# Kernel optimization log

Hardware: AMD Instinct MI355X
Metric: run time of the kernel (lower is better)

## Reference

```python
import jax, jax.numpy as jnp
import numpy as np

D = 768          # wav2vec2-base hidden size
H = 4            # cross-attn heads
HD = D // H
B = 8
N = 1024         # w2v sequence length (target length)
T = 2000         # raw CQCC frames
N_GAT = 3
NUM_CLASSES = 2


def _p(key, shape, scale=0.02):
    return jax.random.normal(key, shape, dtype=jnp.float32) * scale


def layer_norm(x, g, b, eps=1e-5):
    m = x.mean(-1, keepdims=True)
    v = x.var(-1, keepdims=True)
    return (x - m) * jax.lax.rsqrt(v + eps) * g + b


def gelu(x):
    return jax.nn.gelu(x, approximate=False)


def conv1d(x, w, b):
    # x [B,C,T], w [O,I,K], padding=1 (same)
    y = jax.lax.conv_general_dilated(x, w, (1,), [(1, 1)], dimension_numbers=('NCH', 'OIH', 'NCH'))
    return y + b[None, :, None]


def batchnorm(x, g, b, m, v, eps=1e-5):
    # eval-mode BatchNorm1d on [B,C,T]
    return (x - m[None, :, None]) * jax.lax.rsqrt(v[None, :, None] + eps) * g[None, :, None] + b[None, :, None]


def interp_linear(x, target_len):
    # torch F.interpolate(mode='linear', align_corners=False); x [B,T,D] -> [B,target_len,D]
    t_in = x.shape[1]
    pos = (jnp.arange(target_len, dtype=jnp.float32) + 0.5) * (t_in / target_len) - 0.5
    pos = jnp.clip(pos, 0.0, t_in - 1.0)
    lo = jnp.floor(pos).astype(jnp.int32)
    hi = jnp.minimum(lo + 1, t_in - 1)
    w = (pos - lo.astype(jnp.float32))[None, :, None]
    return x[:, lo] * (1.0 - w) + x[:, hi] * w


def mha(q, k, v, in_w, in_b, out_w, out_b):
    # torch nn.MultiheadAttention, batch_first=True
    bb, nq, _ = q.shape
    nk = k.shape[1]
    wq, wk, wv = in_w[:D], in_w[D:2 * D], in_w[2 * D:]
    bq, bk, bv = in_b[:D], in_b[D:2 * D], in_b[2 * D:]
    qh = (q @ wq.T + bq).reshape(bb, nq, H, HD).transpose(0, 2, 1, 3)
    kh = (k @ wk.T + bk).reshape(bb, nk, H, HD).transpose(0, 2, 1, 3)
    vh = (v @ wv.T + bv).reshape(bb, nk, H, HD).transpose(0, 2, 1, 3)
    scores = jnp.einsum('bhqd,bhkd->bhqk', qh, kh) * (1.0 / np.sqrt(HD))
    alpha = jax.nn.softmax(scores, axis=-1)
    o = jnp.einsum('bhqk,bhkd->bhqd', alpha, vh).transpose(0, 2, 1, 3).reshape(bb, nq, D)
    return o @ out_w.T + out_b


def graph_attn(x, fc_w, fc_b, a_w, a_b):
    # GAT score on concat([h_i, h_j]) decomposes additively: e_ij = a_i.h_i + a_j.h_j + b
    h = x @ fc_w.T + fc_b                      # [B,N,D]
    s_i = h @ a_w[:D]                          # [B,N]
    s_j = h @ a_w[D:]                          # [B,N]
    e = s_i[:, :, None] + s_j[:, None, :] + a_b  # [B,N,N]
    alpha = jax.nn.softmax(e, axis=-1)
    return jnp.einsum('bij,bjd->bid', alpha, h)


def _forward(w2v, cqcc, conv1_w, conv1_b, bn1_g, bn1_b, bn1_m, bn1_v,
             conv2_w, conv2_b, bn2_g, bn2_b, bn2_m, bn2_v, pos_embed,
             lnq_g, lnq_b, lnkv_g, lnkv_b,
             a1_in_w, a1_in_b, a1_out_w, a1_out_b,
             a2_in_w, a2_in_b, a2_out_w, a2_out_b,
             gat_fc_w, gat_fc_b, gat_a_w, gat_a_b, gln_g, gln_b,
             clf_w1, clf_b1, clf_w2, clf_b2):
    # CQCC conv stack
    x = gelu(batchnorm(conv1d(cqcc, conv1_w, conv1_b), bn1_g, bn1_b, bn1_m, bn1_v))
    x = gelu(batchnorm(conv1d(x, conv2_w, conv2_b), bn2_g, bn2_b, bn2_m, bn2_v))  # [B,D,T]
    cq = interp_linear(x.transpose(0, 2, 1), w2v.shape[1])  # [B,N,D]
    # shared positional encoding
    n = w2v.shape[1]
    w = w2v + pos_embed[:, :n]
    cq = cq + pos_embed[:, :n]
    # bidirectional cross attention (norm_q / norm_kv shared across directions)
    out1 = mha(layer_norm(cq, lnq_g, lnq_b), layer_norm(w, lnkv_g, lnkv_b),
               layer_norm(w, lnkv_g, lnkv_b), a1_in_w, a1_in_b, a1_out_w, a1_out_b)
    out2 = mha(layer_norm(w, lnq_g, lnq_b), layer_norm(cq, lnkv_g, lnkv_b),
               layer_norm(cq, lnkv_g, lnkv_b), a2_in_w, a2_in_b, a2_out_w, a2_out_b)
    x = out1 + out2
    # 3 residual graph-attention blocks
    for l in range(N_GAT):
        res = x
        x = graph_attn(x, gat_fc_w[l], gat_fc_b[l], gat_a_w[l], gat_a_b[l])
        x = layer_norm(x + res, gln_g[l], gln_b[l])
    pooled = x.mean(axis=1)
    h = gelu(pooled @ clf_w1.T + clf_b1)
    return h @ clf_w2.T + clf_b2


def setup_inputs():
    ks = iter(jax.random.split(jax.random.key(0), 64))
    inp = {}
    inp['w2v'] = jax.random.normal(next(ks), (B, N, D), dtype=jnp.float32)
    inp['cqcc'] = jax.random.normal(next(ks), (B, 20, T), dtype=jnp.float32)
    inp['conv1_w'] = _p(next(ks), (128, 20, 3)); inp['conv1_b'] = jnp.zeros((128,), jnp.float32)
    inp['bn1_g'] = jnp.ones((128,), jnp.float32); inp['bn1_b'] = jnp.zeros((128,), jnp.float32)
    inp['bn1_m'] = jnp.zeros((128,), jnp.float32); inp['bn1_v'] = jnp.ones((128,), jnp.float32)
    inp['conv2_w'] = _p(next(ks), (D, 128, 3)); inp['conv2_b'] = jnp.zeros((D,), jnp.float32)
    inp['bn2_g'] = jnp.ones((D,), jnp.float32); inp['bn2_b'] = jnp.zeros((D,), jnp.float32)
    inp['bn2_m'] = jnp.zeros((D,), jnp.float32); inp['bn2_v'] = jnp.ones((D,), jnp.float32)
    inp['pos_embed'] = _p(next(ks), (1, 2000, D), 1.0)
    inp['lnq_g'] = jnp.ones((D,), jnp.float32); inp['lnq_b'] = jnp.zeros((D,), jnp.float32)
    inp['lnkv_g'] = jnp.ones((D,), jnp.float32); inp['lnkv_b'] = jnp.zeros((D,), jnp.float32)
    inp['a1_in_w'] = _p(next(ks), (3 * D, D)); inp['a1_in_b'] = jnp.zeros((3 * D,), jnp.float32)
    inp['a1_out_w'] = _p(next(ks), (D, D)); inp['a1_out_b'] = jnp.zeros((D,), jnp.float32)
    inp['a2_in_w'] = _p(next(ks), (3 * D, D)); inp['a2_in_b'] = jnp.zeros((3 * D,), jnp.float32)
    inp['a2_out_w'] = _p(next(ks), (D, D)); inp['a2_out_b'] = jnp.zeros((D,), jnp.float32)
    inp['gat_fc_w'] = _p(next(ks), (N_GAT, D, D)); inp['gat_fc_b'] = jnp.zeros((N_GAT, D), jnp.float32)
    inp['gat_a_w'] = _p(next(ks), (N_GAT, 2 * D)); inp['gat_a_b'] = jnp.zeros((N_GAT,), jnp.float32)
    inp['gln_g'] = jnp.ones((N_GAT, D), jnp.float32); inp['gln_b'] = jnp.zeros((N_GAT, D), jnp.float32)
    inp['clf_w1'] = _p(next(ks), (128, D)); inp['clf_b1'] = jnp.zeros((128,), jnp.float32)
    inp['clf_w2'] = _p(next(ks), (NUM_CLASSES, 128)); inp['clf_b2'] = jnp.zeros((NUM_CLASSES,), jnp.float32)
    return inp


def reference(w2v, cqcc, conv1_w, conv1_b, bn1_g, bn1_b, bn1_m, bn1_v,
              conv2_w, conv2_b, bn2_g, bn2_b, bn2_m, bn2_v, pos_embed,
              lnq_g, lnq_b, lnkv_g, lnkv_b,
              a1_in_w, a1_in_b, a1_out_w, a1_out_b,
              a2_in_w, a2_in_b, a2_out_w, a2_out_b,
              gat_fc_w, gat_fc_b, gat_a_w, gat_a_b, gln_g, gln_b,
              clf_w1, clf_b1, clf_w2, clf_b2):
    return _forward(w2v, cqcc, conv1_w, conv1_b, bn1_g, bn1_b, bn1_m, bn1_v,
                    conv2_w, conv2_b, bn2_g, bn2_b, bn2_m, bn2_v, pos_embed,
                    lnq_g, lnq_b, lnkv_g, lnkv_b,
                    a1_in_w, a1_in_b, a1_out_w, a1_out_b,
                    a2_in_w, a2_in_b, a2_out_w, a2_out_b,
                    gat_fc_w, gat_fc_b, gat_a_w, gat_a_b, gln_g, gln_b,
                    clf_w1, clf_b1, clf_w2, clf_b2)
```

## Files before the change

kernel.cpp:

```cpp
#include <hip/hip_runtime.h>
#include <math.h>

#define DD 768
#define NH 4
#define HDIM 192
#define BBATCH 8
#define NSEQ 1024
#define TLEN 2000
#define SLOT 6291456

typedef _Float16 h16;
typedef _Float16 half8v __attribute__((ext_vector_type(8)));
typedef _Float16 half4v __attribute__((ext_vector_type(4)));
typedef float f32x4 __attribute__((ext_vector_type(4)));

__device__ __forceinline__ float gelu_f(float x){
  return 0.5f * x * (1.0f + erff(x * 0.70710678118654752440f));
}
__device__ __forceinline__ float wave_sum(float v){
  #pragma unroll
  for (int off = 32; off; off >>= 1) v += __shfl_xor(v, off);
  return v;
}
__device__ __forceinline__ float wave_max(float v){
  #pragma unroll
  for (int off = 32; off; off >>= 1) v = fmaxf(v, __shfl_xor(v, off));
  return v;
}
__device__ __forceinline__ void gload16(const h16* g, h16* l){
  __builtin_amdgcn_global_load_lds(
      (const __attribute__((address_space(1))) void*)g,
      (__attribute__((address_space(3))) void*)l, 16, 0, 0);
}
__device__ __forceinline__ int xcd_remap(int orig, int nwg){
  int q = nwg >> 3, r = nwg & 7;
  int xcd = orig & 7, idx = orig >> 3;
  return (xcd < r ? xcd * (q + 1) : r * (q + 1) + (xcd - r) * q) + idx;
}

__global__ __launch_bounds__(256) void k_cast(const float* __restrict__ s,
    h16* __restrict__ d, int n){
  int i = blockIdx.x * 256 + threadIdx.x;
  if (i < n) d[i] = (h16)s[i];
}

__global__ __launch_bounds__(256) void k_conv1t(const float* __restrict__ cqcc,
    const float* __restrict__ w, const float* __restrict__ bias,
    const float* __restrict__ g, const float* __restrict__ be,
    const float* __restrict__ mm, const float* __restrict__ vv,
    float* __restrict__ out){
  __shared__ float xs[20][258];
  __shared__ float wsm[32*60];
  const int t0 = blockIdx.x * 256;
  const int ocg = blockIdx.y, b = blockIdx.z;
  const int tid = threadIdx.x;
  for (int idx = tid; idx < 20*258; idx += 256){
    int ic = idx / 258, tt = idx % 258;
    int t = t0 + tt - 1;
    xs[ic][tt] = (t >= 0 && t < TLEN) ? cqcc[((size_t)b*20 + ic)*TLEN + t] : 0.f;
  }
  for (int idx = tid; idx < 32*60; idx += 256)
    wsm[idx] = w[ocg*32*60 + idx];
  __syncthreads();
  int t = t0 + tid;
  if (t >= TLEN) return;
  float acc[32] = {};
  for (int ic = 0; ic < 20; ++ic){
    float x0 = xs[ic][tid], x1v = xs[ic][tid+1], x2v = xs[ic][tid+2];
    #pragma unroll
    for (int oc = 0; oc < 32; ++oc){
      const float* wp = &wsm[(oc*20 + ic)*3];
      acc[oc] += wp[0]*x0 + wp[1]*x1v + wp[2]*x2v;
    }
  }
  #pragma unroll 4
  for (int oc = 0; oc < 32; ++oc){
    int c = ocg*32 + oc;
    float s = rsqrtf(vv[c] + 1e-5f) * g[c];
    float val = (acc[oc] + bias[c] - mm[c]) * s + be[c];
    out[((size_t)b*128 + c)*TLEN + t] = gelu_f(val);
  }
}

__global__ __launch_bounds__(256) void k_im2col(const float* __restrict__ x1,
    h16* __restrict__ A2){
  int idx = blockIdx.x * 256 + threadIdx.x;
  if (idx >= 16000*384) return;
  int c = idx % 384, m = idx / 384;
  int b = m / TLEN, t = m % TLEN;
  int ic = c / 3, kh = c % 3;
  int ts = t + kh - 1;
  float v = (ts < 0 || ts >= TLEN) ? 0.f : x1[((size_t)b*128 + ic)*TLEN + ts];
  A2[idx] = (h16)v;
}

__global__ void k_bnprep(const float* __restrict__ cb, const float* __restrict__ g,
    const float* __restrict__ be, const float* __restrict__ m,
    const float* __restrict__ v, float* __restrict__ sc, float* __restrict__ off){
  int i = blockIdx.x * 256 + threadIdx.x;
  if (i >= DD) return;
  float s = g[i] * rsqrtf(v[i] + 1e-5f);
  sc[i] = s;
  off[i] = (cb[i] - m[i]) * s + be[i];
}

__global__ __launch_bounds__(256) void k_interp_ln(const float* __restrict__ x2,
    const float* __restrict__ pe,
    const float* __restrict__ g1, const float* __restrict__ b1, h16* __restrict__ o1,
    const float* __restrict__ g2, const float* __restrict__ b2, h16* __restrict__ o2){
  __shared__ float ss[4], sqq[4];
  int row = blockIdx.x, tid = threadIdx.x;
  int b = row >> 10, i = row & 1023;
  float p = (i + 0.5f) * ((float)TLEN / (float)NSEQ) - 0.5f;
  p = fminf(fmaxf(p, 0.f), (float)(TLEN - 1));
  int lo = (int)floorf(p);
  int hi = min(lo + 1, TLEN - 1);
  float w = p - (float)lo;
  const float* blo = x2 + ((size_t)b * TLEN + lo) * DD;
  const float* bhi = x2 + ((size_t)b * TLEN + hi) * DD;
  const float* per = pe + (size_t)i * DD;
  float v[3]; float s = 0.f, sq = 0.f;
  #pragma unroll
  for (int j = 0; j < 3; ++j){
    int d = j * 256 + tid;
    float x = blo[d] * (1.f - w) + bhi[d] * w + per[d];
    v[j] = x; s += x; sq += x * x;
  }
  s = wave_sum(s); sq = wave_sum(sq);
  int wv = tid >> 6;
  if ((tid & 63) == 0){ ss[wv] = s; sqq[wv] = sq; }
  __syncthreads();
  s  = ss[0] + ss[1] + ss[2] + ss[3];
  sq = sqq[0] + sqq[1] + sqq[2] + sqq[3];
  float mean = s * (1.f / DD);
  float var  = sq * (1.f / DD) - mean * mean;
  float r = rsqrtf(var + 1e-5f);
  #pragma unroll
  for (int j = 0; j < 3; ++j){
    int d = j * 256 + tid;
    float xn = (v[j] - mean) * r;
    o1[(size_t)row * DD + d] = (h16)(xn * g1[d] + b1[d]);
    o2[(size_t)row * DD + d] = (h16)(xn * g2[d] + b2[d]);
  }
}

__global__ __launch_bounds__(256) void k_addpos_ln(const float* __restrict__ xin,
    const float* __restrict__ pe,
    const float* __restrict__ g1, const float* __restrict__ b1, h16* __restrict__ o1,
    const float* __restrict__ g2, const float* __restrict__ b2, h16* __restrict__ o2){
  __shared__ float ss[4], sqq[4];
  int row = blockIdx.x, tid = threadIdx.x;
  int i = row & 1023;
  const float* ip = xin + (size_t)row * DD;
  const float* per = pe + (size_t)i * DD;
  float v[3]; float s = 0.f, sq = 0.f;
  #pragma unroll
  for (int j = 0; j < 3; ++j){
    int d = j * 256 + tid;
    float x = ip[d] + per[d];
    v[j] = x; s += x; sq += x * x;
  }
  s = wave_sum(s); sq = wave_sum(sq);
  int wv = tid >> 6;
  if ((tid & 63) == 0){ ss[wv] = s; sqq[wv] = sq; }
  __syncthreads();
  s  = ss[0] + ss[1] + ss[2] + ss[3];
  sq = sqq[0] + sqq[1] + sqq[2] + sqq[3];
  float mean = s * (1.f / DD);
  float var  = sq * (1.f / DD) - mean * mean;
  float r = rsqrtf(var + 1e-5f);
  #pragma unroll
  for (int j = 0; j < 3; ++j){
    int d = j * 256 + tid;
    float xn = (v[j] - mean) * r;
    o1[(size_t)row * DD + d] = (h16)(xn * g1[d] + b1[d]);
    o2[(size_t)row * DD + d] = (h16)(xn * g2[d] + b2[d]);
  }
}

__global__ __launch_bounds__(256) void k_ln2(const float* __restrict__ in,
    const float* __restrict__ ctx, const float* __restrict__ g,
    const float* __restrict__ be, float* __restrict__ outf, h16* __restrict__ outh){
  __shared__ float ss[4], sqq[4];
  int row = blockIdx.x, tid = threadIdx.x;
  const float* ip = in + (size_t)row * DD;
  int b = row >> 10;
  float v[3]; float s = 0.f, sq = 0.f;
  #pragma unroll
  for (int j = 0; j < 3; ++j){
    int d = j * 256 + tid;
    float x = ip[d];
    if (ctx) x += ctx[b * DD + d];
    v[j] = x; s += x; sq += x * x;
  }
  s = wave_sum(s); sq = wave_sum(sq);
  int w = tid >> 6;
  if ((tid & 63) == 0){ ss[w] = s; sqq[w] = sq; }
  __syncthreads();
  s  = ss[0] + ss[1] + ss[2] + ss[3];
  sq = sqq[0] + sqq[1] + sqq[2] + sqq[3];
  float mean = s * (1.f / DD);
  float var  = sq * (1.f / DD) - mean * mean;
  float r = rsqrtf(var + 1e-5f);
  #pragma unroll
  for (int j = 0; j < 3; ++j){
    int d = j * 256 + tid;
    float y = (v[j] - mean) * r * g[d] + be[d];
    if (outf) outf[(size_t)row * DD + d] = y;
    if (outh) outh[(size_t)row * DD + d] = (h16)y;
  }
}

#define GEMM_MAINLOOP(Abase, lda, Wbase, ldw, Kdim)                          \
  auto stage = [&](int buf, int kt){                                         \
    _Pragma("unroll")                                                        \
    for (int i = 0; i < 4; ++i){                                             \
      int p = i*256 + tid; int row = p >> 3; int ch = (p & 7) ^ (row & 7);   \
      gload16(Abase + (size_t)(m0+row)*lda + kt + ch*8, &Als[buf][p*8]);     \
    }                                                                        \
    _Pragma("unroll")                                                        \
    for (int i = 0; i < 4; ++i){                                             \
      int p = i*256 + tid; int row = p >> 3; int ch = (p & 7) ^ (row & 7);   \
      gload16(Wbase + (size_t)(n0+row)*ldw + kt + ch*8, &Bls[buf][p*8]);     \
    }                                                                        \
  };                                                                         \
  stage(0, 0);                                                               \
  const int nk = Kdim >> 6;                                                  \
  for (int t = 0; t < nk; ++t){                                              \
    const int cur = t & 1;                                                   \
    if (t + 1 < nk){                                                         \
      stage(cur ^ 1, (t + 1) << 6);                                          \
      asm volatile("s_waitcnt vmcnt(8)" ::: "memory");                       \
    } else {                                                                 \
      asm volatile("s_waitcnt vmcnt(0)" ::: "memory");                       \
    }                                                                        \
    __builtin_amdgcn_s_barrier();                                            \
    __builtin_amdgcn_sched_barrier(0);                                       \
    __builtin_amdgcn_s_setprio(1);                                           \
    _Pragma("unroll")                                                        \
    for (int kk = 0; kk < 2; ++kk){                                          \
      half8v af[4], bf[4];                                                   \
      _Pragma("unroll")                                                      \
      for (int mi = 0; mi < 4; ++mi){                                        \
        int row = wr*64 + mi*16 + lr;                                        \
        int chp = (kk*4 + lg) ^ (row & 7);                                   \
        af[mi] = *(const half8v*)&Als[cur][row*64 + chp*8];                  \
      }                                                                      \
      _Pragma("unroll")                                                      \
      for (int ni = 0; ni < 4; ++ni){                                        \
        int row = wc*64 + ni*16 + lr;                                        \
        int chp = (kk*4 + lg) ^ (row & 7);                                   \
        bf[ni] = *(const half8v*)&Bls[cur][row*64 + chp*8];                  \
      }                                                                      \
      _Pragma("unroll")                                                      \
      for (int mi = 0; mi < 4; ++mi)                                         \
        _Pragma("unroll")                                                    \
        for (int ni = 0; ni < 4; ++ni)                                       \
          acc[mi][ni] = __builtin_amdgcn_mfma_f32_16x16x32_f16(              \
              af[mi], bf[ni], acc[mi][ni], 0, 0, 0);                         \
    }                                                                        \
    __builtin_amdgcn_s_setprio(0);                                           \
    asm volatile("s_waitcnt lgkmcnt(0)" ::: "memory");                       \
    __builtin_amdgcn_sched_barrier(0);                                       \
    __builtin_amdgcn_s_barrier();                                            \
  }

__global__ __launch_bounds__(256) void k_gemm_h(
    const h16* __restrict__ A, const h16* __restrict__ W,
    int lda, int ldw, int ldc, int K,
    const float* __restrict__ bias, const float* __restrict__ sc,
    const float* __restrict__ off, const h16* __restrict__ addh,
    float* __restrict__ outf, h16* __restrict__ outh)
{
  __shared__ h16 Als[2][128*64];
  __shared__ h16 Bls[2][128*64];
  const int tid = threadIdx.x;
  const int gx = gridDim.x, gy = gridDim.y;
  const int wg = xcd_remap(blockIdx.x + gx * blockIdx.y, gx * gy);
  const int n0 = (wg % gx) * 128, m0 = (wg / gx) * 128;
  const int lane = tid & 63, wid = tid >> 6;
  const int wr = wid >> 1, wc = wid & 1;
  const int lr = lane & 15, lg = lane >> 4;
  f32x4 acc[4][4] = {};
  GEMM_MAINLOOP(A, lda, W, ldw, K)
  #pragma unroll
  for (int mi = 0; mi < 4; ++mi){
    #pragma unroll
    for (int ni = 0; ni < 4; ++ni){
      int col = n0 + wc*64 + ni*16 + lr;
      int rowb = m0 + wr*64 + mi*16 + lg*4;
      float cb = bias ? bias[col] : 0.f;
      #pragma unroll
      for (int r = 0; r < 4; ++r){
        size_t idx = (size_t)(rowb + r) * ldc + col;
        float v = acc[mi][ni][r];
        if (sc){ v = v * sc[col] + off[col]; v = gelu_f(v); }
        else v += cb;
        if (addh) v += (float)addh[idx];
        if (outf) outf[idx] = v;
        if (outh) outh[idx] = (h16)v;
      }
    }
  }
}

__global__ __launch_bounds__(256) void k_gemm6(
    const h16* __restrict__ Lall, const h16* __restrict__ w6,
    const float* __restrict__ b1, const float* __restrict__ b2,
    h16* __restrict__ qkv6)
{
  __shared__ h16 Als[2][128*64];
  __shared__ h16 Bls[2][128*64];
  const int tid = threadIdx.x;
  const int gx = gridDim.x, gy = gridDim.y;
  const int nwg = gx * gy * 6;
  const int wg = xcd_remap(blockIdx.x + gx*(blockIdx.y + gy*blockIdx.z), nwg);
  const int n0 = (wg % gx) * 128;
  const int m0 = ((wg / gx) % gy) * 128;
  const int bz = wg / (gx * gy);
  const int aidx = (1468 >> (2*bz)) & 3;
  const h16* A = Lall + (size_t)aidx * SLOT;
  const h16* W = w6 + (size_t)bz * 589824;
  const float* bias = (bz < 3 ? b1 + bz*DD : b2 + (bz-3)*DD);
  h16* C = qkv6 + (size_t)bz * SLOT;
  const int lane = tid & 63, wid = tid >> 6;
  const int wr = wid >> 1, wc = wid & 1;
  const int lr = lane & 15, lg = lane >> 4;
  f32x4 acc[4][4] = {};
  GEMM_MAINLOOP(A, DD, W, DD, DD)
  #pragma unroll
  for (int mi = 0; mi < 4; ++mi){
    #pragma unroll
    for (int ni = 0; ni < 4; ++ni){
      int col = n0 + wc*64 + ni*16 + lr;
      int rowb = m0 + wr*64 + mi*16 + lg*4;
      float cb = bias[col];
      #pragma unroll
      for (int r = 0; r < 4; ++r)
        C[(size_t)(rowb + r) * DD + col] = (h16)(acc[mi][ni][r] + cb);
    }
  }
}

__global__ __launch_bounds__(256) void k_trV(const h16* __restrict__ Vh, int ldv,
    h16* __restrict__ VT){
  __shared__ h16 tile[32][36];
  const int z = blockIdx.z, b = z >> 2, h = z & 3;
  const int q0 = blockIdx.x * 32, d0 = blockIdx.y * 32;
  const int t = threadIdx.x;
  {
    int qq = t >> 3, dg = (t & 7) * 4;
    const h16* src = Vh + ((size_t)b*NSEQ + q0 + qq)*ldv + h*HDIM + d0 + dg;
    half4v v = *(const half4v*)src;
    *(half4v*)&tile[qq][dg] = v;
  }
  __syncthreads();
  {
    int dd = t >> 3, qg = (t & 7) * 4;
    half4v ov;
    ov[0] = tile[qg+0][dd]; ov[1] = tile[qg+1][dd];
    ov[2] = tile[qg+2][dd]; ov[3] = tile[qg+3][dd];
    *(half4v*)(VT + (size_t)z*HDIM*NSEQ + (size_t)(d0+dd)*NSEQ + q0 + qg) = ov;
  }
}

__global__ __launch_bounds__(256) void k_flash(const h16* __restrict__ Qp,
    const h16* __restrict__ Kp, const h16* __restrict__ VTp,
    h16* __restrict__ Op){
  __shared__ h16 Ks[2][32*192];
  __shared__ h16 Vs[2][192*32];
  __shared__ h16 Ps[4][16*32];
  const int tid = threadIdx.x;
  const int bh = blockIdx.x, qt = blockIdx.y;
  const int b = bh >> 2, h = bh & 3;
  const int q0 = qt * 64;
  const h16* Qg = Qp + (size_t)b*NSEQ*DD + h*HDIM;
  const h16* Kg = Kp + (size_t)b*NSEQ*DD + h*HDIM;
  const h16* Vg = VTp + (size_t)bh*HDIM*NSEQ;
  const int lane = tid & 63, wid = tid >> 6;
  const int lr = lane & 15, lg = lane >> 4;
  half8v qf[6];
  {
    int qrow = q0 + wid*16 + lr;
    #pragma unroll
    for (int ks = 0; ks < 6; ++ks)
      qf[ks] = *(const half8v*)(Qg + (size_t)qrow*DD + ks*32 + lg*8);
  }
  auto stageK = [&](int buf, int k0){
    #pragma unroll
    for (int i = 0; i < 3; ++i){
      int p = i*256 + tid;
      int row = p / 24, chp = p % 24;
      int ch = chp ^ (row & 7);
      gload16(Kg + (size_t)(k0+row)*DD + ch*8, &Ks[buf][p*8]);
    }
  };
  auto stageV = [&](int buf, int k0){
    #pragma unroll
    for (int i = 0; i < 3; ++i){
      int p = i*256 + tid;
      int row = p >> 2, chp = p & 3;
      int ch = chp ^ ((row >> 1) & 3);
      gload16(Vg + (size_t)row*NSEQ + k0 + ch*8, &Vs[buf][p*8]);
    }
  };
  stageK(0, 0); stageV(0, 0);
  f32x4 oacc[12] = {};
  float m_run[4] = {-1e30f, -1e30f, -1e30f, -1e30f};
  float l_run[4] = {};
  const float SC = 0.07216878364870322f;
  __syncthreads();
  for (int kt = 0; kt < 32; ++kt){
    const int cur = kt & 1;
    if (kt + 1 < 32){ stageK(cur^1, (kt+1)*32); stageV(cur^1, (kt+1)*32); }
    f32x4 sacc[2] = {};
    __builtin_amdgcn_s_setprio(1);
    #pragma unroll
    for (int ks = 0; ks < 6; ++ks){
      #pragma unroll
      for (int t = 0; t < 2; ++t){
        int krow = t*16 + lr;
        int ch = (ks*4 + lg) ^ (krow & 7);
        half8v kf = *(const half8v*)&Ks[cur][krow*192 + ch*8];
        sacc[t] = __builtin_amdgcn_mfma_f32_16x16x32_f16(qf[ks], kf, sacc[t], 0, 0, 0);
      }
    }
    __builtin_amdgcn_s_setprio(0);
    float mnew[4], c[4], psum[4];
    #pragma unroll
    for (int r = 0; r < 4; ++r){
      float mt = fmaxf(sacc[0][r], sacc[1][r]);
      #pragma unroll
      for (int off = 1; off < 16; off <<= 1) mt = fmaxf(mt, __shfl_xor(mt, off));
      mnew[r] = fmaxf(m_run[r], mt * SC);
      c[r] = __expf(m_run[r] - mnew[r]);
      psum[r] = 0.f;
    }
    #pragma unroll
    for (int t = 0; t < 2; ++t){
      #pragma unroll
      for (int r = 0; r < 4; ++r){
        float p = __expf(sacc[t][r] * SC - mnew[r]);
        psum[r] += p;
        int q = lg*4 + r, key = t*16 + lr;
        int ch = (t*2 + (lr>>3)) ^ ((q>>1) & 3);
        Ps[wid][q*32 + ch*8 + (key & 7)] = (h16)p;
      }
    }
    #pragma unroll
    for (int r = 0; r < 4; ++r){
      #pragma unroll
      for (int off = 1; off < 16; off <<= 1) psum[r] += __shfl_xor(psum[r], off);
      l_run[r] = l_run[r] * c[r] + psum[r];
      m_run[r] = mnew[r];
    }
    #pragma unroll
    for (int dt = 0; dt < 12; ++dt){
      f32x4 o = oacc[dt];
      o[0] *= c[0]; o[1] *= c[1]; o[2] *= c[2]; o[3] *= c[3];
      oacc[dt] = o;
    }
    asm volatile("s_waitcnt lgkmcnt(0)" ::: "memory");
    __builtin_amdgcn_sched_barrier(0);
    {
      int pch = lg ^ ((lr >> 1) & 3);
      half8v pf = *(const half8v*)&Ps[wid][lr*32 + pch*8];
      __builtin_amdgcn_s_setprio(1);
      #pragma unroll
      for (int dt = 0; dt < 12; ++dt){
        int drow = dt*16 + lr;
        int vch = lg ^ ((drow >> 1) & 3);
        half8v vf = *(const half8v*)&Vs[cur][drow*32 + vch*8];
        oacc[dt] = __builtin_amdgcn_mfma_f32_16x16x32_f16(pf, vf, oacc[dt], 0, 0, 0);
      }
      __builtin_amdgcn_s_setprio(0);
    }
    __syncthreads();
  }
  float inv[4];
  #pragma unroll
  for (int r = 0; r < 4; ++r) inv[r] = 1.0f / l_run[r];
  h16* Og = Op + (size_t)b*NSEQ*DD + h*HDIM;
  #pragma unroll
  for (int dt = 0; dt < 12; ++dt){
    #pragma unroll
    for (int r = 0; r < 4; ++r){
      int q = q0 + wid*16 + lg*4 + r;
      Og[(size_t)q*DD + dt*16 + lr] = (h16)(oacc[dt][r] * inv[r]);
    }
  }
}

__global__ __launch_bounds__(128) void k_rowdot(const h16* __restrict__ h,
    const float* __restrict__ aw, float* __restrict__ sj){
  __shared__ float red[2];
  int row = blockIdx.x, tid = threadIdx.x;
  float s = 0.f;
  if (tid < 96){
    half8v v = *(const half8v*)(h + (size_t)row * DD + tid*8);
    #pragma unroll
    for (int j = 0; j < 8; ++j) s += (float)v[j] * aw[tid*8 + j];
  }
  s = wave_sum(s);
  if ((tid & 63) == 0) red[tid >> 6] = s;
  __syncthreads();
  if (tid == 0) sj[row] = red[0] + red[1];
}

__global__ __launch_bounds__(256) void k_softmax1024(const float* __restrict__ x,
    float* __restrict__ y){
  __shared__ float red[4];
  int b = blockIdx.x, tid = threadIdx.x;
  const float* ip = x + b * NSEQ;
  float v[4]; float mx = -1e30f;
  #pragma unroll
  for (int j = 0; j < 4; ++j){ v[j] = ip[j * 256 + tid]; mx = fmaxf(mx, v[j]); }
  mx = wave_max(mx);
  if ((tid & 63) == 0) red[tid >> 6] = mx;
  __syncthreads();
  mx = fmaxf(fmaxf(red[0], red[1]), fmaxf(red[2], red[3]));
  __syncthreads();
  float s = 0.f;
  #pragma unroll
  for (int j = 0; j < 4; ++j){ v[j] = __expf(v[j] - mx); s += v[j]; }
  s = wave_sum(s);
  if ((tid & 63) == 0) red[tid >> 6] = s;
  __syncthreads();
  s = red[0] + red[1] + red[2] + red[3];
  float inv = 1.0f / s;
  #pragma unroll
  for (int j = 0; j < 4; ++j) y[b * NSEQ + j * 256 + tid] = v[j] * inv;
}

__global__ __launch_bounds__(256) void k_ctx1(const float* __restrict__ alpha,
    const h16* __restrict__ h, float* __restrict__ part){
  int d = blockIdx.x * 256 + threadIdx.x;
  int b = blockIdx.y, pc = blockIdx.z;
  if (d >= DD) return;
  float acc = 0.f;
  const h16* hp = h + ((size_t)b * NSEQ + pc * 64) * DD + d;
  const float* ap = alpha + b * NSEQ + pc * 64;
  #pragma unroll 4
  for (int j = 0; j < 64; ++j) acc += ap[j] * (float)hp[(size_t)j * DD];
  part[(size_t)(b * 16 + pc) * DD + d] = acc;
}
__global__ __launch_bounds__(256) void k_ctx2(const float* __restrict__ part,
    float scale, float* __restrict__ ctx){
  int d = blockIdx.x * 256 + threadIdx.x;
  int b = blockIdx.y;
  if (d >= DD) return;
  float acc = 0.f;
  #pragma unroll
  for (int p = 0; p < 16; ++p) acc += part[(size_t)(b * 16 + p) * DD + d];
  ctx[b * DD + d] = acc * scale;
}

__global__ __launch_bounds__(256) void k_pool1(const float* __restrict__ x,
    float* __restrict__ part){
  int d = blockIdx.x * 256 + threadIdx.x;
  int b = blockIdx.y, pc = blockIdx.z;
  if (d >= DD) return;
  float acc = 0.f;
  const float* xp = x + ((size_t)b * NSEQ + pc * 64) * DD + d;
  #pragma unroll 4
  for (int j = 0; j < 64; ++j) acc += xp[(size_t)j * DD];
  part[(size_t)(b * 16 + pc) * DD + d] = acc;
}

__global__ __launch_bounds__(128) void k_clf(const float* __restrict__ pooled,
    const float* __restrict__ w1, const float* __restrict__ b1,
    const float* __restrict__ w2, const float* __restrict__ b2,
    float* __restrict__ out){
  __shared__ float pl[DD];
  __shared__ float h1[128];
  int b = blockIdx.x, tid = threadIdx.x;
  #pragma unroll
  for (int j = 0; j < 6; ++j) pl[j * 128 + tid] = pooled[b * DD + j * 128 + tid];
  __syncthreads();
  float acc = b1[tid];
  const float* wp = w1 + (size_t)tid * DD;
  for (int d = 0; d < DD; ++d) acc += pl[d] * wp[d];
  h1[tid] = gelu_f(acc);
  __syncthreads();
  if (tid < 2){
    float o = b2[tid];
    const float* w2p = w2 + tid * 128;
    for (int c = 0; c < 128; ++c) o += h1[c] * w2p[c];
    out[b * 2 + tid] = o;
  }
}

extern "C" void kernel_launch(void* const* d_in, const int* in_sizes, int n_in,
                              void* d_out, int out_size, void* d_ws, size_t ws_size,
                              hipStream_t stream){
  (void)in_sizes; (void)n_in; (void)out_size;
  const float* w2v      = (const float*)d_in[0];
  const float* cqcc     = (const float*)d_in[1];
  const float* conv1_w  = (const float*)d_in[2];
  const float* conv1_b  = (const float*)d_in[3];
  const float* bn1_g    = (const float*)d_in[4];
  const float* bn1_b    = (const float*)d_in[5];
  const float* bn1_m    = (const float*)d_in[6];
  const float* bn1_v    = (const float*)d_in[7];
  const float* conv2_w  = (const float*)d_in[8];
  const float* conv2_b  = (const float*)d_in[9];
  const float* bn2_g    = (const float*)d_in[10];
  const float* bn2_b    = (const float*)d_in[11];
  const float* bn2_m    = (const float*)d_in[12];
  const float* bn2_v    = (const float*)d_in[13];
  const float* pos_embed= (const float*)d_in[14];
  const float* lnq_g    = (const float*)d_in[15];
  const float* lnq_b    = (const float*)d_in[16];
  const float* lnkv_g   = (const float*)d_in[17];
  const float* lnkv_b   = (const float*)d_in[18];
  const float* a1_in_w  = (const float*)d_in[19];
  const float* a1_in_b  = (const float*)d_in[20];
  const float* a1_out_w = (const float*)d_in[21];
  const float* a1_out_b = (const float*)d_in[22];
  const float* a2_in_w  = (const float*)d_in[23];
  const float* a2_in_b  = (const float*)d_in[24];
  const float* a2_out_w = (const float*)d_in[25];
  const float* a2_out_b = (const float*)d_in[26];
  const float* gat_fc_w = (const float*)d_in[27];
  const float* gat_fc_b = (const float*)d_in[28];
  const float* gat_a_w  = (const float*)d_in[29];
  const float* gln_g    = (const float*)d_in[31];
  const float* gln_b    = (const float*)d_in[32];
  const float* clf_w1   = (const float*)d_in[33];
  const float* clf_b1   = (const float*)d_in[34];
  const float* clf_w2   = (const float*)d_in[35];
  const float* clf_b2   = (const float*)d_in[36];

  char* wsp = (char*)d_ws;
  auto F = [&](size_t bytes){ char* p = wsp; wsp += (bytes + 255) & ~(size_t)255; return p; };
  float* Abuf  = (float*)F(25165824);
  float* Bbuf  = (float*)F(25165824);
  h16* Lall    = (h16*)F(4*12582912);
  h16* qkv6    = (h16*)F(6*12582912);
  h16* VT      = (h16*)F(12582912);
  h16* o1h     = (h16*)F(12582912);
  h16* w6      = (h16*)F(2*3538944);
  h16* w_a1out = (h16*)F(1179648);
  h16* w_a2out = (h16*)F(1179648);
  h16* w_gat   = (h16*)F(3538944);
  h16* w_c2    = (h16*)F(589824);
  float* scb   = (float*)F(3072);
  float* offb  = (float*)F(3072);
  float* sj    = (float*)F(32768);
  float* alpha = (float*)F(32768);
  float* ctxb  = (float*)F(24576);
  float* pooled= (float*)F(24576);
  float* partb = (float*)F(393216);
  if ((size_t)(wsp - (char*)d_ws) > ws_size) return;

  float* x1  = (float*)Lall;
  h16*   A2  = Lall + 2*SLOT;
  float* x2f = (float*)qkv6;
  float* xb  = Abuf;
  h16*   xh  = (h16*)Bbuf;
  h16*   hh  = qkv6;

  const int NR = BBATCH * NSEQ;

  k_cast<<<(1769472+255)/256, 256, 0, stream>>>(a1_in_w,  w6,           1769472);
  k_cast<<<(1769472+255)/256, 256, 0, stream>>>(a2_in_w,  w6 + 1769472, 1769472);
  k_cast<<<(589824+255)/256,  256, 0, stream>>>(a1_out_w, w_a1out, 589824);
  k_cast<<<(589824+255)/256,  256, 0, stream>>>(a2_out_w, w_a2out, 589824);
  k_cast<<<(1769472+255)/256, 256, 0, stream>>>(gat_fc_w, w_gat,   1769472);
  k_cast<<<(294912+255)/256,  256, 0, stream>>>(conv2_w,  w_c2,    294912);
  k_bnprep<<<3, 256, 0, stream>>>(conv2_b, bn2_g, bn2_b, bn2_m, bn2_v, scb, offb);

  k_conv1t<<<dim3(8, 4, BBATCH), 256, 0, stream>>>(cqcc, conv1_w, conv1_b,
      bn1_g, bn1_b, bn1_m, bn1_v, x1);
  k_im2col<<<(16000*384+255)/256, 256, 0, stream>>>(x1, A2);
  k_gemm_h<<<dim3(6, 125), 256, 0, stream>>>(A2, w_c2, 384, 384, DD, 384,
      nullptr, scb, offb, nullptr, x2f, nullptr);

  k_interp_ln<<<NR, 256, 0, stream>>>(x2f, pos_embed,
      lnq_g, lnq_b, Lall, lnkv_g, lnkv_b, Lall + SLOT);
  k_addpos_ln<<<NR, 256, 0, stream>>>(w2v, pos_embed,
      lnq_g, lnq_b, Lall + 2*SLOT, lnkv_g, lnkv_b, Lall + 3*SLOT);

  k_gemm6<<<dim3(6, 64, 6), 256, 0, stream>>>(Lall, w6, a1_in_b, a2_in_b, qkv6);

  dim3 gflash(32, 16);

  k_trV<<<dim3(32, 6, 32), 256, 0, stream>>>(qkv6 + 2*(size_t)SLOT, DD, VT);
  k_flash<<<gflash, 256, 0, stream>>>(qkv6, qkv6 + (size_t)SLOT, VT, qkv6);
  k_gemm_h<<<dim3(6, 64), 256, 0, stream>>>(qkv6, w_a1out, DD, DD, DD, DD,
      a1_out_b, nullptr, nullptr, nullptr, nullptr, o1h);

  k_trV<<<dim3(32, 6, 32), 256, 0, stream>>>(qkv6 + 5*(size_t)SLOT, DD, VT);
  k_flash<<<gflash, 256, 0, stream>>>(qkv6 + 3*(size_t)SLOT, qkv6 + 4*(size_t)SLOT,
                                      VT, qkv6 + 3*(size_t)SLOT);
  k_gemm_h<<<dim3(6, 64), 256, 0, stream>>>(qkv6 + 3*(size_t)SLOT, w_a2out,
      DD, DD, DD, DD, a2_out_b, nullptr, nullptr, o1h, xb, xh);

  for (int l = 0; l < 3; ++l){
    k_gemm_h<<<dim3(6, 64), 256, 0, stream>>>(xh, w_gat + (size_t)l*589824,
        DD, DD, DD, DD, gat_fc_b + l*DD, nullptr, nullptr, nullptr, nullptr, hh);
    k_rowdot<<<NR, 128, 0, stream>>>(hh, gat_a_w + l*2*DD + DD, sj);
    k_softmax1024<<<BBATCH, 256, 0, stream>>>(sj, alpha);
    k_ctx1<<<dim3(3, BBATCH, 16), 256, 0, stream>>>(alpha, hh, partb);
    k_ctx2<<<dim3(3, BBATCH), 256, 0, stream>>>(partb, 1.0f, ctxb);
    k_ln2<<<NR, 256, 0, stream>>>(xb, ctxb, gln_g + l*DD, gln_b + l*DD, xb, xh);
  }

  k_pool1<<<dim3(3, BBATCH, 16), 256, 0, stream>>>(xb, partb);
  k_ctx2<<<dim3(3, BBATCH), 256, 0, stream>>>(partb, 1.0f/NSEQ, pooled);
  k_clf<<<BBATCH, 128, 0, stream>>>(pooled, clf_w1, clf_b1, clf_w2, clf_b2,
                                    (float*)d_out);
}
```

Baseline: 644.5 us.

## Coalesce GEMM, flash and transpose stores via swizzled LDS staging; fp16 conv2 output

GEMM epilogues now stage results through swizzled shared memory and write full 16-byte vectors per row instead of scattered 2/4-byte stores. The flash attention output is likewise staged through LDS per wave. The V transpose uses 64x64 tiles with 16-byte loads and stores. The conv2 GEMM writes fp16 instead of fp32, halving traffic into the interpolation/LayerNorm kernel at some precision cost. The extra barriers and LDS reuse in the flash epilogue add synchronisation risk.

```diff
diff --git a/kernel.cpp b/kernel.cpp
--- a/kernel.cpp
+++ b/kernel.cpp
@@ -104,7 +104,7 @@
   off[i] = (cb[i] - m[i]) * s + be[i];
 }
 
-__global__ __launch_bounds__(256) void k_interp_ln(const float* __restrict__ x2,
+__global__ __launch_bounds__(256) void k_interp_ln(const h16* __restrict__ x2,
     const float* __restrict__ pe,
     const float* __restrict__ g1, const float* __restrict__ b1, h16* __restrict__ o1,
     const float* __restrict__ g2, const float* __restrict__ b2, h16* __restrict__ o2){
@@ -116,14 +116,14 @@
   int lo = (int)floorf(p);
   int hi = min(lo + 1, TLEN - 1);
   float w = p - (float)lo;
-  const float* blo = x2 + ((size_t)b * TLEN + lo) * DD;
-  const float* bhi = x2 + ((size_t)b * TLEN + hi) * DD;
+  const h16* blo = x2 + ((size_t)b * TLEN + lo) * DD;
+  const h16* bhi = x2 + ((size_t)b * TLEN + hi) * DD;
   const float* per = pe + (size_t)i * DD;
   float v[3]; float s = 0.f, sq = 0.f;
   #pragma unroll
   for (int j = 0; j < 3; ++j){
     int d = j * 256 + tid;
-    float x = blo[d] * (1.f - w) + bhi[d] * w + per[d];
+    float x = (float)blo[d] * (1.f - w) + (float)bhi[d] * w + per[d];
     v[j] = x; s += x; sq += x * x;
   }
   s = wave_sum(s); sq = wave_sum(sq);
@@ -211,59 +211,136 @@
   }
 }
 
-#define GEMM_MAINLOOP(Abase, lda, Wbase, ldw, Kdim)                          \
-  auto stage = [&](int buf, int kt){                                         \
-    _Pragma("unroll")                                                        \
-    for (int i = 0; i < 4; ++i){                                             \
-      int p = i*256 + tid; int row = p >> 3; int ch = (p & 7) ^ (row & 7);   \
-      gload16(Abase + (size_t)(m0+row)*lda + kt + ch*8, &Als[buf][p*8]);     \
-    }                                                                        \
-    _Pragma("unroll")                                                        \
-    for (int i = 0; i < 4; ++i){                                             \
-      int p = i*256 + tid; int row = p >> 3; int ch = (p & 7) ^ (row & 7);   \
-      gload16(Wbase + (size_t)(n0+row)*ldw + kt + ch*8, &Bls[buf][p*8]);     \
-    }                                                                        \
-  };                                                                         \
-  stage(0, 0);                                                               \
-  const int nk = Kdim >> 6;                                                  \
-  for (int t = 0; t < nk; ++t){                                              \
-    const int cur = t & 1;                                                   \
-    if (t + 1 < nk){                                                         \
-      stage(cur ^ 1, (t + 1) << 6);                                          \
-      asm volatile("s_waitcnt vmcnt(8)" ::: "memory");                       \
-    } else {                                                                 \
-      asm volatile("s_waitcnt vmcnt(0)" ::: "memory");                       \
-    }                                                                        \
-    __builtin_amdgcn_s_barrier();                                            \
-    __builtin_amdgcn_sched_barrier(0);                                       \
-    __builtin_amdgcn_s_setprio(1);                                           \
-    _Pragma("unroll")                                                        \
-    for (int kk = 0; kk < 2; ++kk){                                          \
-      half8v af[4], bf[4];                                                   \
-      _Pragma("unroll")                                                      \
-      for (int mi = 0; mi < 4; ++mi){                                        \
-        int row = wr*64 + mi*16 + lr;                                        \
-        int chp = (kk*4 + lg) ^ (row & 7);                                   \
-        af[mi] = *(const half8v*)&Als[cur][row*64 + chp*8];                  \
-      }                                                                      \
-      _Pragma("unroll")                                                      \
-      for (int ni = 0; ni < 4; ++ni){                                        \
-        int row = wc*64 + ni*16 + lr;                                        \
-        int chp = (kk*4 + lg) ^ (row & 7);                                   \
-        bf[ni] = *(const half8v*)&Bls[cur][row*64 + chp*8];                  \
-      }                                                                      \
-      _Pragma("unroll")                                                      \
-      for (int mi = 0; mi < 4; ++mi)                                         \
-        _Pragma("unroll")                                                    \
-        for (int ni = 0; ni < 4; ++ni)                                       \
-          acc[mi][ni] = __builtin_amdgcn_mfma_f32_16x16x32_f16(              \
-              af[mi], bf[ni], acc[mi][ni], 0, 0, 0);                         \
-    }                                                                        \
-    __builtin_amdgcn_s_setprio(0);                                           \
-    asm volatile("s_waitcnt lgkmcnt(0)" ::: "memory");                       \
-    __builtin_amdgcn_sched_barrier(0);                                       \
-    __builtin_amdgcn_s_barrier();                                            \
-  }
+__device__ __forceinline__ void gemm_mainloop(const h16* __restrict__ Ab, int lda,
+    const h16* __restrict__ Wb, int ldw, int K, int m0, int n0, int tid,
+    int wr, int wc, int lr, int lg, h16* SH, f32x4 (&acc)[4][4])
+{
+  auto stage = [&](int buf, int kt){
+    #pragma unroll
+    for (int i = 0; i < 4; ++i){
+      int p = i*256 + tid; int row = p >> 3; int ch = (p & 7) ^ (row & 7);
+      gload16(Ab + (size_t)(m0+row)*lda + kt + ch*8, SH + buf*8192 + p*8);
+    }
+    #pragma unroll
+    for (int i = 0; i < 4; ++i){
+      int p = i*256 + tid; int row = p >> 3; int ch = (p & 7) ^ (row & 7);
+      gload16(Wb + (size_t)(n0+row)*ldw + kt + ch*8, SH + 16384 + buf*8192 + p*8);
+    }
+  };
+  stage(0, 0);
+  const int nk = K >> 6;
+  for (int t = 0; t < nk; ++t){
+    const int cur = t & 1;
+    if (t + 1 < nk){
+      stage(cur ^ 1, (t + 1) << 6);
+      asm volatile("s_waitcnt vmcnt(8)" ::: "memory");
+    } else {
+      asm volatile("s_waitcnt vmcnt(0)" ::: "memory");
+    }
+    __builtin_amdgcn_s_barrier();
+    __builtin_amdgcn_sched_barrier(0);
+    __builtin_amdgcn_s_setprio(1);
+    #pragma unroll
+    for (int kk = 0; kk < 2; ++kk){
+      half8v af[4], bf[4];
+      #pragma unroll
+      for (int mi = 0; mi < 4; ++mi){
+        int row = wr*64 + mi*16 + lr;
+        int chp = (kk*4 + lg) ^ (row & 7);
+        af[mi] = *(const half8v*)(SH + cur*8192 + row*64 + chp*8);
+      }
+      #pragma unroll
+      for (int ni = 0; ni < 4; ++ni){
+        int row = wc*64 + ni*16 + lr;
+        int chp = (kk*4 + lg) ^ (row & 7);
+        bf[ni] = *(const half8v*)(SH + 16384 + cur*8192 + row*64 + chp*8);
+      }
+      #pragma unroll
+      for (int mi = 0; mi < 4; ++mi)
+        #pragma unroll
+        for (int ni = 0; ni < 4; ++ni)
+          acc[mi][ni] = __builtin_amdgcn_mfma_f32_16x16x32_f16(
+              af[mi], bf[ni], acc[mi][ni], 0, 0, 0);
+    }
+    __builtin_amdgcn_s_setprio(0);
+    asm volatile("s_waitcnt lgkmcnt(0)" ::: "memory");
+    __builtin_amdgcn_sched_barrier(0);
+    __builtin_amdgcn_s_barrier();
+  }
+}
+
+__device__ __forceinline__ float ep_val(float a, int gr, int gc,
+    const float* bias, const float* sc, const float* off,
+    const h16* addh, int ldc){
+  float v = a;
+  if (sc){ v = v * sc[gc] + off[gc]; v = gelu_f(v); }
+  else if (bias) v += bias[gc];
+  if (addh) v += (float)addh[(size_t)gr * ldc + gc];
+  return v;
+}
+
+__device__ __forceinline__ void ep_store16(h16* SH, f32x4 (&acc)[4][4],
+    int m0, int n0, int tid, int wr, int wc, int lr, int lg,
+    h16* C, int ldc,
+    const float* bias, const float* sc, const float* off, const h16* addh)
+{
+  __syncthreads();
+  #pragma unroll
+  for (int mi = 0; mi < 4; ++mi){
+    #pragma unroll
+    for (int ni = 0; ni < 4; ++ni){
+      int col = wc*64 + ni*16 + lr;
+      int rowb = wr*64 + mi*16 + lg*4;
+      #pragma unroll
+      for (int r = 0; r < 4; ++r){
+        int row = rowb + r;
+        float v = ep_val(acc[mi][ni][r], m0+row, n0+col, bias, sc, off, addh, ldc);
+        int ck = (col >> 3) ^ (row & 7);
+        SH[row*128 + ck*8 + (col & 7)] = (h16)v;
+      }
+    }
+  }
+  __syncthreads();
+  int rrow = tid >> 1, rh = tid & 1;
+  h16* dst = C + (size_t)(m0 + rrow) * ldc + n0 + rh*64;
+  #pragma unroll
+  for (int k = 0; k < 8; ++k){
+    int ck = (rh*8 + k) ^ (rrow & 7);
+    *(half8v*)(dst + k*8) = *(const half8v*)&SH[rrow*128 + ck*8];
+  }
+}
+
+__device__ __forceinline__ void ep_store32(h16* SHh, f32x4 (&acc)[4][4],
+    int m0, int n0, int tid, int wr, int wc, int lr, int lg,
+    float* C, int ldc,
+    const float* bias, const float* sc, const float* off, const h16* addh)
+{
+  float* SF = (float*)SHh;
+  __syncthreads();
+  #pragma unroll
+  for (int mi = 0; mi < 4; ++mi){
+    #pragma unroll
+    for (int ni = 0; ni < 4; ++ni){
+      int col = wc*64 + ni*16 + lr;
+      int rowb = wr*64 + mi*16 + lg*4;
+      #pragma unroll
+      for (int r = 0; r < 4; ++r){
+        int row = rowb + r;
+        float v = ep_val(acc[mi][ni][r], m0+row, n0+col, bias, sc, off, addh, ldc);
+        int ck = (col >> 2) ^ ((row & 7) << 2);
+        SF[row*128 + ck*4 + (col & 3)] = v;
+      }
+    }
+  }
+  __syncthreads();
+  int rrow = tid >> 1, rh = tid & 1;
+  float* dst = C + (size_t)(m0 + rrow) * ldc + n0 + rh*64;
+  #pragma unroll
+  for (int k = 0; k < 16; ++k){
+    int ck = (rh*16 + k) ^ ((rrow & 7) << 2);
+    *(f32x4*)(dst + k*4) = *(const f32x4*)&SF[rrow*128 + ck*4];
+  }
+}
 
 __global__ __launch_bounds__(256) void k_gemm_h(
     const h16* __restrict__ A, const h16* __restrict__ W,
@@ -272,8 +349,7 @@
     const float* __restrict__ off, const h16* __restrict__ addh,
     float* __restrict__ outf, h16* __restrict__ outh)
 {
-  __shared__ h16 Als[2][128*64];
-  __shared__ h16 Bls[2][128*64];
+  __shared__ h16 SH[32768];
   const int tid = threadIdx.x;
   const int gx = gridDim.x, gy = gridDim.y;
   const int wg = xcd_remap(blockIdx.x + gx * blockIdx.y, gx * gy);
@@ -282,26 +358,10 @@
   const int wr = wid >> 1, wc = wid & 1;
   const int lr = lane & 15, lg = lane >> 4;
   f32x4 acc[4][4] = {};
-  GEMM_MAINLOOP(A, lda, W, ldw, K)
-  #pragma unroll
-  for (int mi = 0; mi < 4; ++mi){
-    #pragma unroll
-    for (int ni = 0; ni < 4; ++ni){
-      int col = n0 + wc*64 + ni*16 + lr;
-      int rowb = m0 + wr*64 + mi*16 + lg*4;
-      float cb = bias ? bias[col] : 0.f;
-      #pragma unroll
-      for (int r = 0; r < 4; ++r){
-        size_t idx = (size_t)(rowb + r) * ldc + col;
-        float v = acc[mi][ni][r];
-        if (sc){ v = v * sc[col] + off[col]; v = gelu_f(v); }
-        else v += cb;
-        if (addh) v += (float)addh[idx];
-        if (outf) outf[idx] = v;
-        if (outh) outh[idx] = (h16)v;
-      }
-    }
-  }
+  gemm_mainloop(A, lda, W, ldw, K, m0, n0, tid, wr, wc, lr, lg, SH, acc);
+  ep_store16(SH, acc, m0, n0, tid, wr, wc, lr, lg, outh, ldc, bias, sc, off, addh);
+  if (outf)
+    ep_store32(SH, acc, m0, n0, tid, wr, wc, lr, lg, outf, ldc, bias, sc, off, addh);
 }
 
 __global__ __launch_bounds__(256) void k_gemm6(
@@ -309,8 +369,7 @@
     const float* __restrict__ b1, const float* __restrict__ b2,
     h16* __restrict__ qkv6)
 {
-  __shared__ h16 Als[2][128*64];
-  __shared__ h16 Bls[2][128*64];
+  __shared__ h16 SH[32768];
   const int tid = threadIdx.x;
   const int gx = gridDim.x, gy = gridDim.y;
   const int nwg = gx * gy * 6;
@@ -327,40 +386,39 @@
   const int wr = wid >> 1, wc = wid & 1;
   const int lr = lane & 15, lg = lane >> 4;
   f32x4 acc[4][4] = {};
-  GEMM_MAINLOOP(A, DD, W, DD, DD)
-  #pragma unroll
-  for (int mi = 0; mi < 4; ++mi){
-    #pragma unroll
-    for (int ni = 0; ni < 4; ++ni){
-      int col = n0 + wc*64 + ni*16 + lr;
-      int rowb = m0 + wr*64 + mi*16 + lg*4;
-      float cb = bias[col];
-      #pragma unroll
-      for (int r = 0; r < 4; ++r)
-        C[(size_t)(rowb + r) * DD + col] = (h16)(acc[mi][ni][r] + cb);
-    }
-  }
+  gemm_mainloop(A, DD, W, DD, DD, m0, n0, tid, wr, wc, lr, lg, SH, acc);
+  ep_store16(SH, acc, m0, n0, tid, wr, wc, lr, lg, C, DD,
+             bias, nullptr, nullptr, nullptr);
 }
 
 __global__ __launch_bounds__(256) void k_trV(const h16* __restrict__ Vh, int ldv,
     h16* __restrict__ VT){
-  __shared__ h16 tile[32][36];
+  __shared__ h16 tile[64*64];
   const int z = blockIdx.z, b = z >> 2, h = z & 3;
-  const int q0 = blockIdx.x * 32, d0 = blockIdx.y * 32;
+  const int q0 = blockIdx.x * 64, d0 = blockIdx.y * 64;
   const int t = threadIdx.x;
   {
-    int qq = t >> 3, dg = (t & 7) * 4;
-    const h16* src = Vh + ((size_t)b*NSEQ + q0 + qq)*ldv + h*HDIM + d0 + dg;
-    half4v v = *(const half4v*)src;
-    *(half4v*)&tile[qq][dg] = v;
+    int qq = t >> 2, ds = (t & 3) * 16;
+    const h16* src = Vh + ((size_t)b*NSEQ + q0 + qq)*ldv + h*HDIM + d0 + ds;
+    half8v v0 = *(const half8v*)src;
+    half8v v1 = *(const half8v*)(src + 8);
+    int c0 = (ds >> 3) ^ (qq & 7), c1 = ((ds >> 3) + 1) ^ (qq & 7);
+    *(half8v*)&tile[qq*64 + c0*8] = v0;
+    *(half8v*)&tile[qq*64 + c1*8] = v1;
   }
   __syncthreads();
   {
-    int dd = t >> 3, qg = (t & 7) * 4;
-    half4v ov;
-    ov[0] = tile[qg+0][dd]; ov[1] = tile[qg+1][dd];
-    ov[2] = tile[qg+2][dd]; ov[3] = tile[qg+3][dd];
-    *(half4v*)(VT + (size_t)z*HDIM*NSEQ + (size_t)(d0+dd)*NSEQ + q0 + qg) = ov;
+    int dd = t >> 2, qs = (t & 3) * 16;
+    half8v o0, o1;
+    #pragma unroll
+    for (int j = 0; j < 8; ++j){
+      int q = qs + j, q2 = qs + 8 + j;
+      o0[j] = tile[q*64  + (((dd>>3) ^ (q&7))*8)  + (dd & 7)];
+      o1[j] = tile[q2*64 + (((dd>>3) ^ (q2&7))*8) + (dd & 7)];
+    }
+    h16* dst = VT + (size_t)z*HDIM*NSEQ + (size_t)(d0+dd)*NSEQ + q0 + qs;
+    *(half8v*)dst = o0;
+    *(half8v*)(dst + 8) = o1;
   }
 }
 
@@ -480,13 +538,26 @@
   float inv[4];
   #pragma unroll
   for (int r = 0; r < 4; ++r) inv[r] = 1.0f / l_run[r];
-  h16* Og = Op + (size_t)b*NSEQ*DD + h*HDIM;
+  h16* cl = &Ks[0][0] + wid * (16*192);
   #pragma unroll
   for (int dt = 0; dt < 12; ++dt){
     #pragma unroll
     for (int r = 0; r < 4; ++r){
-      int q = q0 + wid*16 + lg*4 + r;
-      Og[(size_t)q*DD + dt*16 + lr] = (h16)(oacc[dt][r] * inv[r]);
+      int q = lg*4 + r, col = dt*16 + lr;
+      int ck = (col >> 3) ^ (q & 7);
+      cl[q*192 + ck*8 + (col & 7)] = (h16)(oacc[dt][r] * inv[r]);
+    }
+  }
+  asm volatile("s_waitcnt lgkmcnt(0)" ::: "memory");
+  __builtin_amdgcn_sched_barrier(0);
+  {
+    int row = lane >> 2, seg = lane & 3;
+    int qg = q0 + wid*16 + row;
+    h16* og = Op + (size_t)b*NSEQ*DD + (size_t)qg*DD + h*HDIM + seg*48;
+    #pragma unroll
+    for (int c = 0; c < 6; ++c){
+      int ck = (seg*6 + c) ^ (row & 7);
+      *(half8v*)(og + c*8) = *(const half8v*)&cl[row*192 + ck*8];
     }
   }
 }
@@ -655,7 +726,7 @@
 
   float* x1  = (float*)Lall;
   h16*   A2  = Lall + 2*SLOT;
-  float* x2f = (float*)qkv6;
+  h16*   x2h = qkv6;
   float* xb  = Abuf;
   h16*   xh  = (h16*)Bbuf;
   h16*   hh  = qkv6;
@@ -674,9 +745,9 @@
       bn1_g, bn1_b, bn1_m, bn1_v, x1);
   k_im2col<<<(16000*384+255)/256, 256, 0, stream>>>(x1, A2);
   k_gemm_h<<<dim3(6, 125), 256, 0, stream>>>(A2, w_c2, 384, 384, DD, 384,
-      nullptr, scb, offb, nullptr, x2f, nullptr);
-
-  k_interp_ln<<<NR, 256, 0, stream>>>(x2f, pos_embed,
+      nullptr, scb, offb, nullptr, nullptr, x2h);
+
+  k_interp_ln<<<NR, 256, 0, stream>>>(x2h, pos_embed,
       lnq_g, lnq_b, Lall, lnkv_g, lnkv_b, Lall + SLOT);
   k_addpos_ln<<<NR, 256, 0, stream>>>(w2v, pos_embed,
       lnq_g, lnq_b, Lall + 2*SLOT, lnkv_g, lnkv_b, Lall + 3*SLOT);
@@ -685,12 +756,12 @@
 
   dim3 gflash(32, 16);
 
-  k_trV<<<dim3(32, 6, 32), 256, 0, stream>>>(qkv6 + 2*(size_t)SLOT, DD, VT);
+  k_trV<<<dim3(16, 3, 32), 256, 0, stream>>>(qkv6 + 2*(size_t)SLOT, DD, VT);
   k_flash<<<gflash, 256, 0, stream>>>(qkv6, qkv6 + (size_t)SLOT, VT, qkv6);
   k_gemm_h<<<dim3(6, 64), 256, 0, stream>>>(qkv6, w_a1out, DD, DD, DD, DD,
       a1_out_b, nullptr, nullptr, nullptr, nullptr, o1h);
 
-  k_trV<<<dim3(32, 6, 32), 256, 0, stream>>>(qkv6 + 5*(size_t)SLOT, DD, VT);
+  k_trV<<<dim3(16, 3, 32), 256, 0, stream>>>(qkv6 + 5*(size_t)SLOT, DD, VT);
   k_flash<<<gflash, 256, 0, stream>>>(qkv6 + 3*(size_t)SLOT, qkv6 + 4*(size_t)SLOT,
                                       VT, qkv6 + 3*(size_t)SLOT);
   k_gemm_h<<<dim3(6, 64), 256, 0, stream>>>(qkv6 + 3*(size_t)SLOT, w_a2out,
```

Result: slower. 734.6 us (+14.0%).
